# Optimization experiments

Hardware: AMD Instinct MI355X
Metric: run time of the kernel (lower is better)

## Reference

```python
import jax, jax.numpy as jnp
import numpy as np


def setup_inputs() -> dict:
    key = jax.random.key(0)
    k1, k2, k3 = jax.random.split(key, 3)
    B, C, H, W = 64, 2048, 14, 14
    M, NC = 32, 396
    x = jax.random.normal(k1, (B, C, H, W), dtype=jnp.float32)
    Wa = jax.random.normal(k2, (M, C), dtype=jnp.float32) * (1.0 / np.sqrt(C))
    ba = jnp.zeros((M,), dtype=jnp.float32)
    Wc = jax.random.normal(k3, (NC, M * C), dtype=jnp.float32) * (1.0 / np.sqrt(M * C))
    bc = jnp.zeros((NC,), dtype=jnp.float32)
    return {"x": x, "Wa": Wa, "ba": ba, "Wc": Wc, "bc": bc}


def reference(x, Wa, ba, Wc, bc):
    # x: [B, C, H, W]
    B, C, H, W = x.shape
    M = Wa.shape[0]
    # 1x1 conv == channel contraction; attention maps [B, M, H, W]
    A = jax.nn.sigmoid(jnp.einsum('bchw,mc->bmhw', x, Wa) + ba[None, :, None, None])
    # BAP: per-head attention-weighted global average pool -> [B, M, C]
    bap = jnp.einsum('bchw,bmhw->bmc', x, A) / (H * W)
    feats = bap.reshape(B, M * C)  # concat head-major, matching torch cat order
    return feats @ Wc.T + bc
```

## Files before the change

### kernel.cpp

```cpp
#include <hip/hip_runtime.h>
#include <hip/hip_bf16.h>
#include <cstdint>

#define B_N 64
#define C_N 2048
#define HW_N 196
#define HWP 224
#define M_N 32
#define NC_N 396
#define K_N 65536

typedef __attribute__((ext_vector_type(8))) short bf16x8;
typedef __attribute__((ext_vector_type(4))) float f32x4;

__device__ inline short f2bf(float x) {
  union { float f; unsigned u; } v; v.f = x;
  unsigned r = (v.u + 0x7FFFu + ((v.u >> 16) & 1u)) >> 16;
  return (short)r;
}

__global__ __launch_bounds__(256) void k1_attn(
    const float* __restrict__ x, const float* __restrict__ Wa,
    const float* __restrict__ ba, short* __restrict__ Apad) {
  __shared__ float red[4][8][64];
  const int t = threadIdx.x;
  const int w = t >> 6, lane = t & 63, lq = lane >> 4, ln = lane & 15;
  const int b = blockIdx.y;
  const int hw0 = blockIdx.x * 16;
  const int hwl = hw0 + ln;
  const int hwc = hwl < HW_N ? hwl : HW_N - 1;
  const float* __restrict__ xb  = x + (size_t)b * (C_N * HW_N) + hwc;
  const float* __restrict__ wa0 = Wa + (size_t)ln * C_N;
  const float* __restrict__ wa1 = Wa + (size_t)(16 + ln) * C_N;

  f32x4 d0 = {0.f, 0.f, 0.f, 0.f}, d1 = {0.f, 0.f, 0.f, 0.f};
  const int cw = w * 512 + lq * 8;
#pragma unroll 2
  for (int s = 0; s < 16; ++s) {
    const int cc = cw + s * 32;
    float4 a0l = *(const float4*)(wa0 + cc);
    float4 a0h = *(const float4*)(wa0 + cc + 4);
    float4 a1l = *(const float4*)(wa1 + cc);
    float4 a1h = *(const float4*)(wa1 + cc + 4);
    bf16x8 af0, af1, bfr;
    af0[0]=f2bf(a0l.x); af0[1]=f2bf(a0l.y); af0[2]=f2bf(a0l.z); af0[3]=f2bf(a0l.w);
    af0[4]=f2bf(a0h.x); af0[5]=f2bf(a0h.y); af0[6]=f2bf(a0h.z); af0[7]=f2bf(a0h.w);
    af1[0]=f2bf(a1l.x); af1[1]=f2bf(a1l.y); af1[2]=f2bf(a1l.z); af1[3]=f2bf(a1l.w);
    af1[4]=f2bf(a1h.x); af1[5]=f2bf(a1h.y); af1[6]=f2bf(a1h.z); af1[7]=f2bf(a1h.w);
#pragma unroll
    for (int j = 0; j < 8; ++j)
      bfr[j] = f2bf(xb[(size_t)(cc + j) * HW_N]);
    d0 = __builtin_amdgcn_mfma_f32_16x16x32_bf16(af0, bfr, d0, 0, 0, 0);
    d1 = __builtin_amdgcn_mfma_f32_16x16x32_bf16(af1, bfr, d1, 0, 0, 0);
  }
  red[w][0][lane] = d0[0]; red[w][1][lane] = d0[1];
  red[w][2][lane] = d0[2]; red[w][3][lane] = d0[3];
  red[w][4][lane] = d1[0]; red[w][5][lane] = d1[1];
  red[w][6][lane] = d1[2]; red[w][7][lane] = d1[3];
  __syncthreads();
#pragma unroll
  for (int rep = 0; rep < 2; ++rep) {
    int id = t + rep * 256;
    int lr = id >> 3, fr = id & 7;
    float ssum = red[0][fr][lr] + red[1][fr][lr] + red[2][fr][lr] + red[3][fr][lr];
    int m  = (fr >> 2) * 16 + (lr >> 4) * 4 + (fr & 3);
    int hw = hw0 + (lr & 15);
    float zz = ssum + ba[m];
    float av = (hw < HW_N) ? 1.f / (1.f + __expf(-zz)) : 0.f;
    Apad[((size_t)b * M_N + m) * HWP + hw] = f2bf(av);
  }
}

__global__ __launch_bounds__(256) void k2_bap(
    const float* __restrict__ x, const short* __restrict__ Apad,
    short* __restrict__ featsb) {
  const int t = threadIdx.x;
  const int w = t >> 6, lane = t & 63, lq = lane >> 4, ln = lane & 15;
  const int b = blockIdx.y;
  const int c = blockIdx.x * 64 + w * 16 + ln;
  const float* __restrict__ xrow = x + (size_t)b * (C_N * HW_N) + (size_t)c * HW_N;
  const short* __restrict__ ap0 = Apad + ((size_t)b * M_N + ln) * HWP + lq * 8;
  const short* __restrict__ ap1 = ap0 + 16 * HWP;

  f32x4 d0 = {0.f, 0.f, 0.f, 0.f}, d1 = {0.f, 0.f, 0.f, 0.f};
#pragma unroll
  for (int s = 0; s < 7; ++s) {
    bf16x8 a0 = *(const bf16x8*)(ap0 + s * 32);
    bf16x8 a1 = *(const bf16x8*)(ap1 + s * 32);
    bf16x8 bfr;
    const int h = s * 32 + lq * 8;
    if (s < 6) {
      float4 b0 = *(const float4*)(xrow + h);
      float4 b1 = *(const float4*)(xrow + h + 4);
      bfr[0]=f2bf(b0.x); bfr[1]=f2bf(b0.y); bfr[2]=f2bf(b0.z); bfr[3]=f2bf(b0.w);
      bfr[4]=f2bf(b1.x); bfr[5]=f2bf(b1.y); bfr[6]=f2bf(b1.z); bfr[7]=f2bf(b1.w);
    } else {
      float4 b0 = make_float4(0.f, 0.f, 0.f, 0.f);
      if (lq == 0) b0 = *(const float4*)(xrow + h);
      bfr[0]=f2bf(b0.x); bfr[1]=f2bf(b0.y); bfr[2]=f2bf(b0.z); bfr[3]=f2bf(b0.w);
      bfr[4]=0; bfr[5]=0; bfr[6]=0; bfr[7]=0;
    }
    d0 = __builtin_amdgcn_mfma_f32_16x16x32_bf16(a0, bfr, d0, 0, 0, 0);
    d1 = __builtin_amdgcn_mfma_f32_16x16x32_bf16(a1, bfr, d1, 0, 0, 0);
  }
  const float sc = 1.f / (float)HW_N;
  short* fb = featsb + (size_t)b * K_N + c;
#pragma unroll
  for (int r = 0; r < 4; ++r) {
    int m0 = lq * 4 + r;
    fb[(size_t)m0 * C_N]        = f2bf(d0[r] * sc);
    fb[(size_t)(16 + m0) * C_N] = f2bf(d1[r] * sc);
  }
}

__global__ __launch_bounds__(256) void k3_cls(
    const short* __restrict__ featsb, const float* __restrict__ Wc,
    float* __restrict__ partial) {
  const int t = threadIdx.x;
  const int w = t >> 6, lane = t & 63, lq = lane >> 4, ln = lane & 15;
  const int n = blockIdx.x * 64 + w * 16 + ln;
  const int nc = n < NC_N ? n : NC_N - 1;
  const size_t k0 = (size_t)blockIdx.y * 512;
  const float* __restrict__ wrow = Wc + (size_t)nc * K_N + k0 + lq * 8;
  const short* __restrict__ f0 = featsb + k0 + lq * 8 + (size_t)ln * K_N;

  f32x4 acc0 = {0.f,0.f,0.f,0.f}, acc1 = {0.f,0.f,0.f,0.f};
  f32x4 acc2 = {0.f,0.f,0.f,0.f}, acc3 = {0.f,0.f,0.f,0.f};
#pragma unroll 4
  for (int s = 0; s < 16; ++s) {
    const int kk = s * 32;
    float4 w0 = *(const float4*)(wrow + kk);
    float4 w1 = *(const float4*)(wrow + kk + 4);
    bf16x8 bfr;
    bfr[0]=f2bf(w0.x); bfr[1]=f2bf(w0.y); bfr[2]=f2bf(w0.z); bfr[3]=f2bf(w0.w);
    bfr[4]=f2bf(w1.x); bfr[5]=f2bf(w1.y); bfr[6]=f2bf(w1.z); bfr[7]=f2bf(w1.w);
    bf16x8 a0 = *(const bf16x8*)(f0 + kk);
    bf16x8 a1 = *(const bf16x8*)(f0 + (size_t)16 * K_N + kk);
    bf16x8 a2 = *(const bf16x8*)(f0 + (size_t)32 * K_N + kk);
    bf16x8 a3 = *(const bf16x8*)(f0 + (size_t)48 * K_N + kk);
    acc0 = __builtin_amdgcn_mfma_f32_16x16x32_bf16(a0, bfr, acc0, 0, 0, 0);
    acc1 = __builtin_amdgcn_mfma_f32_16x16x32_bf16(a1, bfr, acc1, 0, 0, 0);
    acc2 = __builtin_amdgcn_mfma_f32_16x16x32_bf16(a2, bfr, acc2, 0, 0, 0);
    acc3 = __builtin_amdgcn_mfma_f32_16x16x32_bf16(a3, bfr, acc3, 0, 0, 0);
  }
  if (n < NC_N) {
    float* po = partial + (size_t)blockIdx.y * (B_N * NC_N) + n;
#pragma unroll
    for (int r = 0; r < 4; ++r) {
      int br = lq * 4 + r;
      po[(size_t)br * NC_N]        = acc0[r];
      po[(size_t)(16 + br) * NC_N] = acc1[r];
      po[(size_t)(32 + br) * NC_N] = acc2[r];
      po[(size_t)(48 + br) * NC_N] = acc3[r];
    }
  }
}

__global__ __launch_bounds__(256) void k4_reduce(
    const float* __restrict__ partial, const float* __restrict__ bc,
    float* __restrict__ out) {
  int idx = blockIdx.x * 256 + threadIdx.x;
  if (idx >= B_N * NC_N) return;
  int n = idx % NC_N;
  float s = bc[n];
#pragma unroll 8
  for (int kc = 0; kc < 128; ++kc) s += partial[(size_t)kc * (B_N * NC_N) + idx];
  out[idx] = s;
}

extern "C" void kernel_launch(void* const* d_in, const int* in_sizes, int n_in,
                              void* d_out, int out_size, void* d_ws, size_t ws_size,
                              hipStream_t stream) {
  const float* x  = (const float*)d_in[0];
  const float* Wa = (const float*)d_in[1];
  const float* ba = (const float*)d_in[2];
  const float* Wc = (const float*)d_in[3];
  const float* bc = (const float*)d_in[4];
  float* out = (float*)d_out;

  char* wsb = (char*)d_ws;
  short* Apad    = (short*)(wsb);
  short* featsb  = (short*)(wsb + (1u  << 20));
  float* partial = (float*)(wsb + (10u << 20));
  (void)ws_size; (void)in_sizes; (void)n_in; (void)out_size;

  hipLaunchKernelGGL(k1_attn, dim3(14, 64), dim3(256), 0, stream,
                     x, Wa, ba, Apad);
  hipLaunchKernelGGL(k2_bap, dim3(32, 64), dim3(256), 0, stream,
                     x, Apad, featsb);
  hipLaunchKernelGGL(k3_cls, dim3(7, 128), dim3(256), 0, stream,
                     featsb, Wc, partial);
  hipLaunchKernelGGL(k4_reduce, dim3(99), dim3(256), 0, stream,
                     partial, bc, out);
}
```

Before: 298.4 us.

## Restructure attention conv as split-C LDS-tiled MFMA with separate sigmoid reduce

```diff
diff --git a/kernel.cpp b/kernel.cpp
--- a/kernel.cpp
+++ b/kernel.cpp
@@ -9,6 +9,9 @@
 #define M_N 32
 #define NC_N 396
 #define K_N 65536
+#define CCH 256
+#define NCH 8
+#define ZSTRIDE (B_N * M_N * HW_N)
 
 typedef __attribute__((ext_vector_type(8))) short bf16x8;
 typedef __attribute__((ext_vector_type(4))) float f32x4;
@@ -19,56 +22,133 @@
   return (short)r;
 }
 
-__global__ __launch_bounds__(256) void k1_attn(
+__device__ inline unsigned packbf2(float lo, float hi) {
+  return ((unsigned)(unsigned short)f2bf(hi) << 16) |
+         (unsigned)(unsigned short)f2bf(lo);
+}
+
+__global__ __launch_bounds__(256) void k1a_partial(
     const float* __restrict__ x, const float* __restrict__ Wa,
-    const float* __restrict__ ba, short* __restrict__ Apad) {
-  __shared__ float red[4][8][64];
+    float* __restrict__ z) {
+  __shared__ short waT[32][264];
+  __shared__ short xT[208][40];
   const int t = threadIdx.x;
   const int w = t >> 6, lane = t & 63, lq = lane >> 4, ln = lane & 15;
-  const int b = blockIdx.y;
-  const int hw0 = blockIdx.x * 16;
-  const int hwl = hw0 + ln;
-  const int hwc = hwl < HW_N ? hwl : HW_N - 1;
-  const float* __restrict__ xb  = x + (size_t)b * (C_N * HW_N) + hwc;
-  const float* __restrict__ wa0 = Wa + (size_t)ln * C_N;
-  const float* __restrict__ wa1 = Wa + (size_t)(16 + ln) * C_N;
-
-  f32x4 d0 = {0.f, 0.f, 0.f, 0.f}, d1 = {0.f, 0.f, 0.f, 0.f};
-  const int cw = w * 512 + lq * 8;
-#pragma unroll 2
-  for (int s = 0; s < 16; ++s) {
-    const int cc = cw + s * 32;
-    float4 a0l = *(const float4*)(wa0 + cc);
-    float4 a0h = *(const float4*)(wa0 + cc + 4);
-    float4 a1l = *(const float4*)(wa1 + cc);
-    float4 a1h = *(const float4*)(wa1 + cc + 4);
-    bf16x8 af0, af1, bfr;
-    af0[0]=f2bf(a0l.x); af0[1]=f2bf(a0l.y); af0[2]=f2bf(a0l.z); af0[3]=f2bf(a0l.w);
-    af0[4]=f2bf(a0h.x); af0[5]=f2bf(a0h.y); af0[6]=f2bf(a0h.z); af0[7]=f2bf(a0h.w);
-    af1[0]=f2bf(a1l.x); af1[1]=f2bf(a1l.y); af1[2]=f2bf(a1l.z); af1[3]=f2bf(a1l.w);
-    af1[4]=f2bf(a1h.x); af1[5]=f2bf(a1h.y); af1[6]=f2bf(a1h.z); af1[7]=f2bf(a1h.w);
-#pragma unroll
-    for (int j = 0; j < 8; ++j)
-      bfr[j] = f2bf(xb[(size_t)(cc + j) * HW_N]);
-    d0 = __builtin_amdgcn_mfma_f32_16x16x32_bf16(af0, bfr, d0, 0, 0, 0);
-    d1 = __builtin_amdgcn_mfma_f32_16x16x32_bf16(af1, bfr, d1, 0, 0, 0);
-  }
-  red[w][0][lane] = d0[0]; red[w][1][lane] = d0[1];
-  red[w][2][lane] = d0[2]; red[w][3][lane] = d0[3];
-  red[w][4][lane] = d1[0]; red[w][5][lane] = d1[1];
-  red[w][6][lane] = d1[2]; red[w][7][lane] = d1[3];
-  __syncthreads();
-#pragma unroll
-  for (int rep = 0; rep < 2; ++rep) {
-    int id = t + rep * 256;
-    int lr = id >> 3, fr = id & 7;
-    float ssum = red[0][fr][lr] + red[1][fr][lr] + red[2][fr][lr] + red[3][fr][lr];
-    int m  = (fr >> 2) * 16 + (lr >> 4) * 4 + (fr & 3);
-    int hw = hw0 + (lr & 15);
-    float zz = ssum + ba[m];
-    float av = (hw < HW_N) ? 1.f / (1.f + __expf(-zz)) : 0.f;
-    Apad[((size_t)b * M_N + m) * HWP + hw] = f2bf(av);
-  }
+  const int cx = blockIdx.x, b = blockIdx.y;
+  const int c0 = cx * CCH;
+
+  unsigned* xTw = (unsigned*)xT;
+  if (t < 240) xTw[196 * 20 + t] = 0u;
+  for (int i = t; i < 2048; i += 256) {
+    int m = i >> 6, f4 = i & 63;
+    float4 v = *(const float4*)(Wa + (size_t)m * C_N + c0 + f4 * 4);
+    uint2 pk;
+    pk.x = packbf2(v.x, v.y);
+    pk.y = packbf2(v.z, v.w);
+    *(uint2*)((char*)waT + m * 528 + f4 * 8) = pk;
+  }
+
+  f32x4 acc[4][2];
+#pragma unroll
+  for (int ti = 0; ti < 4; ++ti) {
+    acc[ti][0] = (f32x4){0.f, 0.f, 0.f, 0.f};
+    acc[ti][1] = (f32x4){0.f, 0.f, 0.f, 0.f};
+  }
+
+  const float* __restrict__ xb0 = x + (size_t)b * (C_N * HW_N) + (size_t)c0 * HW_N;
+  const int p0 = t & 15;
+  const int q0 = t >> 4;
+
+  for (int ss = 0; ss < 8; ++ss) {
+    const float* xs = xb0 + (size_t)ss * 32 * HW_N;
+    {
+      const float* r0 = xs + (2 * p0) * HW_N + 4 * q0;
+      float4 fa0 = *(const float4*)r0;
+      float4 fb0 = *(const float4*)(r0 + HW_N);
+      float4 fa1 = *(const float4*)(r0 + 64);
+      float4 fb1 = *(const float4*)(r0 + 64 + HW_N);
+      float4 fa2 = *(const float4*)(r0 + 128);
+      float4 fb2 = *(const float4*)(r0 + 128 + HW_N);
+      unsigned* d0 = xTw + q0 * 80 + p0;
+      d0[0]  = packbf2(fa0.x, fb0.x);
+      d0[20] = packbf2(fa0.y, fb0.y);
+      d0[40] = packbf2(fa0.z, fb0.z);
+      d0[60] = packbf2(fa0.w, fb0.w);
+      unsigned* d1 = d0 + 1280;
+      d1[0]  = packbf2(fa1.x, fb1.x);
+      d1[20] = packbf2(fa1.y, fb1.y);
+      d1[40] = packbf2(fa1.z, fb1.z);
+      d1[60] = packbf2(fa1.w, fb1.w);
+      unsigned* d2 = d0 + 2560;
+      d2[0]  = packbf2(fa2.x, fb2.x);
+      d2[20] = packbf2(fa2.y, fb2.y);
+      d2[40] = packbf2(fa2.z, fb2.z);
+      d2[60] = packbf2(fa2.w, fb2.w);
+      if (t < 16) {
+        const float* r3 = xs + (2 * t) * HW_N + 192;
+        float4 fa3 = *(const float4*)r3;
+        float4 fb3 = *(const float4*)(r3 + HW_N);
+        unsigned* d3 = xTw + 48 * 80 + t;
+        d3[0]  = packbf2(fa3.x, fb3.x);
+        d3[20] = packbf2(fa3.y, fb3.y);
+        d3[40] = packbf2(fa3.z, fb3.z);
+        d3[60] = packbf2(fa3.w, fb3.w);
+      }
+    }
+    __syncthreads();
+    const int kb = ss * 64 + lq * 16;
+    bf16x8 af0 = *(const bf16x8*)((const char*)waT + ln * 528 + kb);
+    bf16x8 af1 = *(const bf16x8*)((const char*)waT + (16 + ln) * 528 + kb);
+#pragma unroll
+    for (int ti = 0; ti < 4; ++ti) {
+      int ht = w + ti * 4;
+      if (ht < 13) {
+        bf16x8 bfr = *(const bf16x8*)((const char*)xT + (ht * 16 + ln) * 80 + lq * 16);
+        acc[ti][0] = __builtin_amdgcn_mfma_f32_16x16x32_bf16(af0, bfr, acc[ti][0], 0, 0, 0);
+        acc[ti][1] = __builtin_amdgcn_mfma_f32_16x16x32_bf16(af1, bfr, acc[ti][1], 0, 0, 0);
+      }
+    }
+    __syncthreads();
+  }
+
+  float* zc = z + (size_t)(cx * B_N + b) * (M_N * HW_N);
+#pragma unroll
+  for (int ti = 0; ti < 4; ++ti) {
+    int ht = w + ti * 4;
+    if (ht < 13) {
+      int hw = ht * 16 + ln;
+      if (hw < HW_N) {
+#pragma unroll
+        for (int mt = 0; mt < 2; ++mt) {
+#pragma unroll
+          for (int r = 0; r < 4; ++r) {
+            int m = mt * 16 + lq * 4 + r;
+            zc[(size_t)m * HW_N + hw] = acc[ti][mt][r];
+          }
+        }
+      }
+    }
+  }
+}
+
+__global__ __launch_bounds__(256) void k1b_sig(
+    const float* __restrict__ z, const float* __restrict__ ba,
+    short* __restrict__ Apad) {
+  int idx = blockIdx.x * 256 + threadIdx.x;
+  int b = idx / (M_N * HWP);
+  int r = idx - b * (M_N * HWP);
+  int m = r / HWP;
+  int hw = r - m * HWP;
+  short out = 0;
+  if (hw < HW_N) {
+    float s = ba[m];
+    size_t base = ((size_t)b * M_N + m) * HW_N + hw;
+#pragma unroll
+    for (int cx = 0; cx < NCH; ++cx)
+      s += z[(size_t)cx * ZSTRIDE + base];
+    out = f2bf(1.f / (1.f + __expf(-s)));
+  }
+  Apad[idx] = out;
 }
 
 __global__ __launch_bounds__(256) void k2_bap(
@@ -182,10 +262,13 @@
   short* Apad    = (short*)(wsb);
   short* featsb  = (short*)(wsb + (1u  << 20));
   float* partial = (float*)(wsb + (10u << 20));
+  float* zbuf    = (float*)(wsb + (10u << 20));
   (void)ws_size; (void)in_sizes; (void)n_in; (void)out_size;
 
-  hipLaunchKernelGGL(k1_attn, dim3(14, 64), dim3(256), 0, stream,
-                     x, Wa, ba, Apad);
+  hipLaunchKernelGGL(k1a_partial, dim3(NCH, B_N), dim3(256), 0, stream,
+                     x, Wa, zbuf);
+  hipLaunchKernelGGL(k1b_sig, dim3(1792), dim3(256), 0, stream,
+                     zbuf, ba, Apad);
   hipLaunchKernelGGL(k2_bap, dim3(32, 64), dim3(256), 0, stream,
                      x, Apad, featsb);
   hipLaunchKernelGGL(k3_cls, dim3(7, 128), dim3(256), 0, stream,
```

Result: faster. 284.5 us (-4.7%).
